# Kernel tuning notes

Measured on AMD Instinct MI355X. Metric: run time of the kernel, lower is better.

## Reference

```python
import jax, jax.numpy as jnp
import numpy as np

LATENT, D_MODEL, WIN, ENC_IN, BATCH = 128, 512, 256, 55, 256


def setup_inputs() -> dict:
    key = jax.random.key(0)
    ks = jax.random.split(key, 9)
    sl = lambda k, shape, fan_in: (jax.random.normal(k, shape, jnp.float32) / np.sqrt(fan_in)).astype(jnp.float32)
    return {
        "z": jax.random.normal(ks[0], (BATCH, LATENT), jnp.float32),
        "h_proj_w": sl(ks[1], (D_MODEL, LATENT), LATENT),
        "h_proj_b": sl(ks[2], (D_MODEL,), LATENT),
        "w_ih": sl(ks[3], (3 * D_MODEL, D_MODEL), D_MODEL),
        "w_hh": sl(ks[4], (3 * D_MODEL, D_MODEL), D_MODEL),
        "b_ih": sl(ks[5], (3 * D_MODEL,), D_MODEL),
        "b_hh": sl(ks[6], (3 * D_MODEL,), D_MODEL),
        "out_w": sl(ks[7], (ENC_IN, D_MODEL), D_MODEL),
        "out_b": sl(ks[8], (ENC_IN,), D_MODEL),
        "win_size": WIN,
    }


def reference(z, h_proj_w, h_proj_b, w_ih, w_hh, b_ih, b_hh, out_w, out_b, win_size):
    d = h_proj_w.shape[0]
    # h0 = tanh(Linear(z)) -> [B, d]
    h0 = jnp.tanh(z @ h_proj_w.T + h_proj_b)
    # GRU input is all zeros, so input-gate preactivation is just b_ih
    # (w_ih @ 0 == 0); gate order in torch GRU is (r, z, n).
    gi_r, gi_z, gi_n = b_ih[:d], b_ih[d:2 * d], b_ih[2 * d:]

    def step(h, _):
        gh = h @ w_hh.T + b_hh                      # [B, 3d]
        r = jax.nn.sigmoid(gi_r + gh[:, :d])
        zg = jax.nn.sigmoid(gi_z + gh[:, d:2 * d])
        n = jnp.tanh(gi_n + r * gh[:, 2 * d:])
        h_new = (1.0 - zg) * n + zg * h
        return h_new, h_new

    _, hs = jax.lax.scan(step, h0, None, length=win_size)  # [T, B, d]
    hs = jnp.transpose(hs, (1, 0, 2))                      # [B, T, d]
    return hs @ out_w.T + out_b                            # [B, T, enc_in]
```

## Files before the change

kernel.cpp:

```cpp
#include <hip/hip_runtime.h>

#define DM     512
#define LAT    128
#define WIN_   256
#define ENC    55
#define GB     32
#define BT     8
#define DS     64
#define TPB    768
#define OUT_T  256
#define AROW16 528
#define GHS    200
#define OWS    520
#define NK     22
#define NKP    24

typedef __attribute__((ext_vector_type(8))) short bf8;
typedef __attribute__((ext_vector_type(4))) float f4;
typedef unsigned long long u64;
typedef unsigned short u16;

__device__ __align__(128) u64 g_ring2[2][GB][8][BT][NKP];
__device__ __align__(128) u64 g_lcnt[GB * 8 * 16];

__device__ __forceinline__ u16 f2bf(float f) {
    union { float f; unsigned int i; } v; v.f = f;
    unsigned int r = v.i + 0x7fffu + ((v.i >> 16) & 1u);
    return (u16)(r >> 16);
}
__device__ __forceinline__ float sigm(float x) { return 1.f / (1.f + __expf(-x)); }
__device__ __forceinline__ float tanh_(float x) {
    x = fminf(x, 40.f);
    float e = __expf(2.f * x);
    return (e - 1.f) / (e + 1.f);
}
#define ALOAD(p)     __hip_atomic_load((p),      __ATOMIC_RELAXED, __HIP_MEMORY_SCOPE_AGENT)
#define ASTORE(p, v) __hip_atomic_store((p), (v), __ATOMIC_RELAXED, __HIP_MEMORY_SCOPE_AGENT)

template <bool DUP>
__device__ __forceinline__ void fetch_slice(const u64* rb, u16 want, u16* sm,
                                            u16* sm2, int j, int lane) {
    const int row = lane >> 3, k = lane & 7;
    {
        const u64* pp = rb + 7 * NKP + 21;
        long guard = 0;
        while ((u16)ALOAD(pp) != want && guard < (1L << 18)) ++guard;
    }
    const u64* p0 = rb + row * NKP + k;
    const bool v2 = (k + 16) < NK;
    u64 r0 = ALOAD(p0), r1 = ALOAD(p0 + 8), r2 = v2 ? ALOAD(p0 + 16) : 0;
    bool ok0 = ((u16)r0 == want), ok1 = ((u16)r1 == want),
         ok2 = (!v2) || ((u16)r2 == want);
    long guard = 0;
    while (!__all(ok0 && ok1 && ok2) && guard < (1L << 18)) {
        if (!ok0) { r0 = ALOAD(p0);      ok0 = ((u16)r0 == want); }
        if (!ok1) { r1 = ALOAD(p0 + 8);  ok1 = ((u16)r1 == want); }
        if (!ok2) { r2 = ALOAD(p0 + 16); ok2 = ((u16)r2 == want); }
        ++guard;
    }
    u16* dst  = sm  + row * AROW16 + j * 64;
    u16* dst2 = sm2 + row * AROW16 + j * 64;
    int db = 3 * k;
    dst[db] = (u16)(r0 >> 16); dst[db + 1] = (u16)(r0 >> 32); dst[db + 2] = (u16)(r0 >> 48);
    if (DUP) { dst2[db] = (u16)(r0 >> 16); dst2[db + 1] = (u16)(r0 >> 32); dst2[db + 2] = (u16)(r0 >> 48); }
    db = 3 * (k + 8);
    dst[db] = (u16)(r1 >> 16); dst[db + 1] = (u16)(r1 >> 32); dst[db + 2] = (u16)(r1 >> 48);
    if (DUP) { dst2[db] = (u16)(r1 >> 16); dst2[db + 1] = (u16)(r1 >> 32); dst2[db + 2] = (u16)(r1 >> 48); }
    if (v2) {
        db = 3 * (k + 16);
        dst[db] = (u16)(r2 >> 16);
        if (DUP) dst2[db] = (u16)(r2 >> 16);
        if (db + 1 < DS) { dst[db + 1] = (u16)(r2 >> 32); if (DUP) dst2[db + 1] = (u16)(r2 >> 32); }
        if (db + 2 < DS) { dst[db + 2] = (u16)(r2 >> 48); if (DUP) dst2[db + 2] = (u16)(r2 >> 48); }
    }
}

__global__ __launch_bounds__(TPB, 3) void gru_fused(
    const float* __restrict__ z,
    const float* __restrict__ hpw,
    const float* __restrict__ hpb,
    const float* __restrict__ whh,
    const float* __restrict__ bih,
    const float* __restrict__ bhh,
    const float* __restrict__ outw,
    const float* __restrict__ outb,
    float* __restrict__ out)
{
    const int blk  = blockIdx.x;
    const int g    = blk & (GB - 1);
    const int s    = blk >> 5;
    const int d0   = s * DS;
    const int row0 = g * BT;
    const int tid  = threadIdx.x;
    const int wave = tid >> 6;
    const int lane = tid & 63;
    const int quad = lane >> 4;
    const int nl   = lane & 15;

    __shared__ __align__(16) u16 sm16[BT * AROW16];
    __shared__ __align__(16) u16 pbuf[BT * AROW16];
    __shared__ __align__(16) float ghT[BT][GHS];
    __shared__ float bias_r[DS], bias_z[DS], gin_[DS], bhn_[DS];
    __shared__ __align__(16) u16 hpack[BT][66];
    __shared__ __align__(16) u16 sOutW[ENC * OWS];
    __shared__ float sOutB[64];
    __shared__ u64 sh_lc;

    u64* lc_own = g_lcnt + (u64)(g * 8 + s) * 16;
    if (tid == 0) sh_lc = ALOAD(lc_own);

    if (tid < DS) {
        int dg = d0 + tid;
        bias_r[tid] = bih[dg]       + bhh[dg];
        bias_z[tid] = bih[512 + dg] + bhh[512 + dg];
        gin_[tid]   = bih[1024 + dg];
        bhn_[tid]   = bhh[1024 + dg];
    }
    if (tid < ENC) sOutB[tid] = outb[tid];
    for (int i = tid; i < ENC * DM; i += TPB)
        sOutW[(i >> 9) * OWS + (i & 511)] = f2bf(outw[i]);

    const int gl   = wave * 16 + nl;
    const int sel  = gl >> 6;
    const int jrow = sel * 512 + d0 + (gl & 63);
    bf8 bfrag[16];
#pragma unroll
    for (int kb = 0; kb < 16; ++kb) {
        const float* wp = whh + jrow * DM + kb * 32 + quad * 8;
        bf8 v;
#pragma unroll
        for (int j = 0; j < 8; ++j) v[j] = (short)f2bf(wp[j]);
        bfrag[kb] = v;
    }
    __syncthreads();

    const u64 base = sh_lc * 512ULL + 1ULL;
    float hprev_reg = 0.f;

    if (wave < BT) {
        float acc = hpb[d0 + lane];
        const float* zr = z + (row0 + wave) * LAT;
        const float* wr = hpw + (d0 + lane) * LAT;
#pragma unroll 8
        for (int k = 0; k < LAT; ++k) acc += zr[k] * wr[k];
        hprev_reg = tanh_(acc);
        if (lane < 2) hpack[wave][64 + lane] = 0;
        hpack[wave][lane] = f2bf(hprev_reg);
        const u16 sq = (u16)base;
        if (lane < NK) {
            u16 b0 = hpack[wave][3 * lane], b1 = hpack[wave][3 * lane + 1],
                b2 = hpack[wave][3 * lane + 2];
            u64 rec = (u64)sq | ((u64)b0 << 16) | ((u64)b1 << 32) | ((u64)b2 << 48);
            ASTORE(&g_ring2[0][g][s][wave][lane], rec);
        }
    }

    const u16* afrag_base = sm16 + (nl & 7) * AROW16;
    const u16* pfrag_base = pbuf + (nl & 7) * AROW16;

    for (int t = 1; t <= WIN_; ++t) {
        const int sp = (t - 1) & 1, sc = t & 1;
        const u16 want = (u16)(base + t - 1);
        const int tau  = t - 2;
        const bool proj = (tau >= 0) && ((tau & 7) == s);

        if (wave < BT) {
            u16 hb = f2bf(hprev_reg);
            sm16[wave * AROW16 + d0 + lane] = hb;
            if (proj) pbuf[wave * AROW16 + d0 + lane] = hb;
        }
        if (wave >= 1 && wave < 8) {
            const int j = (s + wave) & 7;
            if (proj) fetch_slice<true >(&g_ring2[sp][g][j][0][0], want, sm16, pbuf, j, lane);
            else      fetch_slice<false>(&g_ring2[sp][g][j][0][0], want, sm16, pbuf, j, lane);
        }
        __syncthreads();

        f4 acc = {0.f, 0.f, 0.f, 0.f};
#pragma unroll
        for (int kb = 0; kb < 16; ++kb) {
            bf8 av = *(const bf8*)(afrag_base + quad * 8 + kb * 32);
            acc = __builtin_amdgcn_mfma_f32_16x16x32_bf16(av, bfrag[kb], acc, 0, 0, 0);
        }
        if (quad < 2) {
#pragma unroll
            for (int r = 0; r < 4; ++r) ghT[quad * 4 + r][gl] = acc[r];
        }
        __syncthreads();

        if (wave < BT) {
            const int d = lane;
            const float* grow = &ghT[wave][0];
            float rr = sigm(bias_r[d] + grow[d]);
            float zg = sigm(bias_z[d] + grow[64 + d]);
            float nn = tanh_(gin_[d] + rr * (bhn_[d] + grow[128 + d]));
            float h  = (1.f - zg) * nn + zg * hprev_reg;
            hprev_reg = h;
            hpack[wave][d] = f2bf(h);
            const u16 sq = (u16)(base + t);
            if (lane < NK) {
                u16 b0 = hpack[wave][3 * lane], b1 = hpack[wave][3 * lane + 1],
                    b2 = hpack[wave][3 * lane + 2];
                u64 rec = (u64)sq | ((u64)b0 << 16) | ((u64)b1 << 32) | ((u64)b2 << 48);
                ASTORE(&g_ring2[sc][g][s][wave][lane], rec);
            }
        }

        if (proj && wave >= 8) {
            const int e  = (wave - 8) * 16 + nl;
            const int ec = (e < ENC) ? e : (ENC - 1);
            const u16* wrow = sOutW + ec * OWS + quad * 8;
            f4 accp = {0.f, 0.f, 0.f, 0.f};
#pragma unroll
            for (int kb = 0; kb < 16; ++kb) {
                bf8 av = *(const bf8*)(pfrag_base + quad * 8 + kb * 32);
                bf8 wv = *(const bf8*)(wrow + kb * 32);
                accp = __builtin_amdgcn_mfma_f32_16x16x32_bf16(av, wv, accp, 0, 0, 0);
            }
            if (quad < 2 && e < ENC) {
                float ob = sOutB[e];
#pragma unroll
                for (int r = 0; r < 4; ++r) {
                    int m = quad * 4 + r;
                    out[(row0 + m) * (OUT_T * ENC) + tau * ENC + e] = accp[r] + ob;
                }
            }
        }
    }

    if (s == 7) {
        const u16 want = (u16)(base + WIN_);
        if (wave < BT)
            sm16[wave * AROW16 + d0 + lane] = f2bf(hprev_reg);
        if (wave >= 1 && wave < 8) {
            const int j = (s + wave) & 7;
            fetch_slice<false>(&g_ring2[0][g][j][0][0], want, sm16, pbuf, j, lane);
        }
        __syncthreads();
        if (wave >= 8) {
            const int e  = (wave - 8) * 16 + nl;
            const int ec = (e < ENC) ? e : (ENC - 1);
            const u16* wrow = sOutW + ec * OWS + quad * 8;
            f4 accp = {0.f, 0.f, 0.f, 0.f};
#pragma unroll
            for (int kb = 0; kb < 16; ++kb) {
                bf8 av = *(const bf8*)(afrag_base + quad * 8 + kb * 32);
                bf8 wv = *(const bf8*)(wrow + kb * 32);
                accp = __builtin_amdgcn_mfma_f32_16x16x32_bf16(av, wv, accp, 0, 0, 0);
            }
            if (quad < 2 && e < ENC) {
                float ob = sOutB[e];
#pragma unroll
                for (int r = 0; r < 4; ++r) {
                    int m = quad * 4 + r;
                    out[(row0 + m) * (OUT_T * ENC) + 255 * ENC + e] = accp[r] + ob;
                }
            }
        }
    }

    if (tid == 0) ASTORE(lc_own, sh_lc + 1ULL);
}

extern "C" void kernel_launch(void* const* d_in, const int* in_sizes, int n_in,
                              void* d_out, int out_size, void* d_ws, size_t ws_size,
                              hipStream_t stream) {
    const float* z    = (const float*)d_in[0];
    const float* hpw  = (const float*)d_in[1];
    const float* hpb  = (const float*)d_in[2];
    const float* whh  = (const float*)d_in[4];
    const float* bih  = (const float*)d_in[5];
    const float* bhh  = (const float*)d_in[6];
    const float* outw = (const float*)d_in[7];
    const float* outb = (const float*)d_in[8];
    float* out = (float*)d_out;

    (void)d_ws; (void)ws_size;
    gru_fused<<<dim3(256), dim3(TPB), 0, stream>>>(
        z, hpw, hpb, whh, bih, bhh, outw, outb, out);
}
```

Measured before the change: 717.2 us.

## Drop duplicate projection buffer and pipeline spin-wait loads on ring flag

```diff
diff --git a/kernel.cpp b/kernel.cpp
--- a/kernel.cpp
+++ b/kernel.cpp
@@ -37,14 +37,17 @@
 #define ALOAD(p)     __hip_atomic_load((p),      __ATOMIC_RELAXED, __HIP_MEMORY_SCOPE_AGENT)
 #define ASTORE(p, v) __hip_atomic_store((p), (v), __ATOMIC_RELAXED, __HIP_MEMORY_SCOPE_AGENT)
 
-template <bool DUP>
 __device__ __forceinline__ void fetch_slice(const u64* rb, u16 want, u16* sm,
-                                            u16* sm2, int j, int lane) {
+                                            int j, int lane) {
     const int row = lane >> 3, k = lane & 7;
     {
         const u64* pp = rb + 7 * NKP + 21;
+        u64 q0 = ALOAD(pp), q1 = ALOAD(pp), q2 = ALOAD(pp), q3 = ALOAD(pp);
         long guard = 0;
-        while ((u16)ALOAD(pp) != want && guard < (1L << 18)) ++guard;
+        while ((u16)q0 != want && guard < (1L << 18)) {
+            q0 = q1; q1 = q2; q2 = q3; q3 = ALOAD(pp);
+            ++guard;
+        }
     }
     const u64* p0 = rb + row * NKP + k;
     const bool v2 = (k + 16) < NK;
@@ -58,20 +61,16 @@
         if (!ok2) { r2 = ALOAD(p0 + 16); ok2 = ((u16)r2 == want); }
         ++guard;
     }
-    u16* dst  = sm  + row * AROW16 + j * 64;
-    u16* dst2 = sm2 + row * AROW16 + j * 64;
+    u16* dst = sm + row * AROW16 + j * 64;
     int db = 3 * k;
     dst[db] = (u16)(r0 >> 16); dst[db + 1] = (u16)(r0 >> 32); dst[db + 2] = (u16)(r0 >> 48);
-    if (DUP) { dst2[db] = (u16)(r0 >> 16); dst2[db + 1] = (u16)(r0 >> 32); dst2[db + 2] = (u16)(r0 >> 48); }
     db = 3 * (k + 8);
     dst[db] = (u16)(r1 >> 16); dst[db + 1] = (u16)(r1 >> 32); dst[db + 2] = (u16)(r1 >> 48);
-    if (DUP) { dst2[db] = (u16)(r1 >> 16); dst2[db + 1] = (u16)(r1 >> 32); dst2[db + 2] = (u16)(r1 >> 48); }
     if (v2) {
         db = 3 * (k + 16);
         dst[db] = (u16)(r2 >> 16);
-        if (DUP) dst2[db] = (u16)(r2 >> 16);
-        if (db + 1 < DS) { dst[db + 1] = (u16)(r2 >> 32); if (DUP) dst2[db + 1] = (u16)(r2 >> 32); }
-        if (db + 2 < DS) { dst[db + 2] = (u16)(r2 >> 48); if (DUP) dst2[db + 2] = (u16)(r2 >> 48); }
+        if (db + 1 < DS) dst[db + 1] = (u16)(r2 >> 32);
+        if (db + 2 < DS) dst[db + 2] = (u16)(r2 >> 48);
     }
 }
 
@@ -98,7 +97,6 @@
     const int nl   = lane & 15;
 
     __shared__ __align__(16) u16 sm16[BT * AROW16];
-    __shared__ __align__(16) u16 pbuf[BT * AROW16];
     __shared__ __align__(16) float ghT[BT][GHS];
     __shared__ float bias_r[DS], bias_z[DS], gin_[DS], bhn_[DS];
     __shared__ __align__(16) u16 hpack[BT][66];
@@ -156,23 +154,16 @@
     }
 
     const u16* afrag_base = sm16 + (nl & 7) * AROW16;
-    const u16* pfrag_base = pbuf + (nl & 7) * AROW16;
 
     for (int t = 1; t <= WIN_; ++t) {
         const int sp = (t - 1) & 1, sc = t & 1;
         const u16 want = (u16)(base + t - 1);
-        const int tau  = t - 2;
-        const bool proj = (tau >= 0) && ((tau & 7) == s);
-
-        if (wave < BT) {
-            u16 hb = f2bf(hprev_reg);
-            sm16[wave * AROW16 + d0 + lane] = hb;
-            if (proj) pbuf[wave * AROW16 + d0 + lane] = hb;
-        }
+
+        if (wave < BT)
+            sm16[wave * AROW16 + d0 + lane] = f2bf(hprev_reg);
         if (wave >= 1 && wave < 8) {
             const int j = (s + wave) & 7;
-            if (proj) fetch_slice<true >(&g_ring2[sp][g][j][0][0], want, sm16, pbuf, j, lane);
-            else      fetch_slice<false>(&g_ring2[sp][g][j][0][0], want, sm16, pbuf, j, lane);
+            fetch_slice(&g_ring2[sp][g][j][0][0], want, sm16, j, lane);
         }
         __syncthreads();
 
@@ -206,6 +197,8 @@
             }
         }
 
+        const int tau = t - 2;
+        const bool proj = (tau >= 0) && ((tau & 7) == s);
         if (proj && wave >= 8) {
             const int e  = (wave - 8) * 16 + nl;
             const int ec = (e < ENC) ? e : (ENC - 1);
@@ -213,7 +206,7 @@
             f4 accp = {0.f, 0.f, 0.f, 0.f};
 #pragma unroll
             for (int kb = 0; kb < 16; ++kb) {
-                bf8 av = *(const bf8*)(pfrag_base + quad * 8 + kb * 32);
+                bf8 av = *(const bf8*)(afrag_base + quad * 8 + kb * 32);
                 bf8 wv = *(const bf8*)(wrow + kb * 32);
                 accp = __builtin_amdgcn_mfma_f32_16x16x32_bf16(av, wv, accp, 0, 0, 0);
             }
@@ -226,6 +219,7 @@
                 }
             }
         }
+        if (proj) __syncthreads();
     }
 
     if (s == 7) {
@@ -234,7 +228,7 @@
             sm16[wave * AROW16 + d0 + lane] = f2bf(hprev_reg);
         if (wave >= 1 && wave < 8) {
             const int j = (s + wave) & 7;
-            fetch_slice<false>(&g_ring2[0][g][j][0][0], want, sm16, pbuf, j, lane);
+            fetch_slice(&g_ring2[0][g][j][0][0], want, sm16, j, lane);
         }
         __syncthreads();
         if (wave >= 8) {
```

After: 759.8 us. +5.9%, slower.
